# Optimization experiments

Hardware: AMD Instinct MI355X
Metric: run time of the kernel (lower is better)

The kernel has to match this reference:

```python
import jax, jax.numpy as jnp
import numpy as np

D = 1024      # in_features
H = 8         # heads per branch (head_num // 2)
DH = (D // 2) // H  # 64
OUT = 1024

def _split_heads(x, B, S):
    # [B, S, D/2] -> [B, H, S, DH]
    return x.reshape(B, S, H, DH).transpose(0, 2, 1, 3)

def _attn(q, k, v):
    # q,k,v: [B, H, S, DH]
    scores = jnp.einsum('bhqd,bhkd->bhqk', q, k) / jnp.sqrt(jnp.float32(DH))
    a = jax.nn.softmax(scores, axis=-1)
    return jnp.einsum('bhqk,bhkd->bhqd', a, v)

def setup_inputs() -> dict:
    key = jax.random.key(0)
    ks = jax.random.split(key, 16)
    B, S = 2, 2048
    d2 = D // 2
    sc = lambda fan_in: 1.0 / np.sqrt(fan_in)
    inp = {
        'f1': jax.random.normal(ks[0], (B, S, D), jnp.float32),
        'f2': jax.random.normal(ks[1], (B, S, D), jnp.float32),
    }
    names = ['qs', 'ks', 'vs', 'qc', 'kc', 'vc']
    for i, n in enumerate(names):
        inp['W' + n] = jax.random.uniform(ks[2 + i], (d2, D), jnp.float32, -sc(D), sc(D))
        inp['b' + n] = jax.random.uniform(ks[8 + i], (d2,), jnp.float32, -sc(D), sc(D))
    inp['Wo'] = jax.random.uniform(ks[14], (OUT, 2 * D), jnp.float32, -sc(2 * D), sc(2 * D))
    inp['bo'] = jax.random.uniform(ks[15], (OUT,), jnp.float32, -sc(2 * D), sc(2 * D))
    return inp

def reference(f1, f2, Wqs, bqs, Wks, bks, Wvs, bvs, Wqc, bqc, Wkc, bkc, Wvc, bvc, Wo, bo):
    B, S, _ = f1.shape
    lin = lambda x, W, b: jax.nn.relu(x @ W.T + b)
    qs = lin(f1, Wqs, bqs); ks_ = lin(f1, Wks, bks); vs = lin(f1, Wvs, bvs)
    qc = lin(f1, Wqc, bqc); kc = lin(f2, Wkc, bkc); vc = lin(f2, Wvc, bvc)
    ys = _attn(_split_heads(qs, B, S), _split_heads(ks_, B, S), _split_heads(vs, B, S))
    yc = _attn(_split_heads(qc, B, S), _split_heads(kc, B, S), _split_heads(vc, B, S))
    merge = lambda y: y.transpose(0, 2, 1, 3).reshape(B, S, D // 2)
    # reshape_to_batches followed by reshape_from_batches on vs/vc is identity
    y = jnp.concatenate([merge(ys), merge(yc), vs, vc], axis=-1)  # [B, S, 2D]
    return jax.nn.relu(y @ Wo.T + bo)
```

## Files before the change

kernel.cpp:

```cpp
#include <hip/hip_runtime.h>
#include <hip/hip_bf16.h>

using bf16 = __hip_bfloat16;
typedef __attribute__((ext_vector_type(8))) short bf16x8;
typedef __attribute__((ext_vector_type(4))) float f32x4;
typedef __attribute__((ext_vector_type(16))) float f32x16;
typedef __attribute__((ext_vector_type(4))) unsigned int u32x4;

#define MTOT 4096

__device__ __forceinline__ f32x4 fzero() {
    f32x4 z = {0.f, 0.f, 0.f, 0.f};
    return z;
}
__device__ __forceinline__ f32x16 fzero16() {
    f32x16 z = {0.f,0.f,0.f,0.f,0.f,0.f,0.f,0.f,0.f,0.f,0.f,0.f,0.f,0.f,0.f,0.f};
    return z;
}

__device__ __forceinline__ f32x4 mfma16(bf16x8 a, bf16x8 b, f32x4 c) {
    return __builtin_amdgcn_mfma_f32_16x16x32_bf16(a, b, c, 0, 0, 0);
}
__device__ __forceinline__ f32x16 mfma32(bf16x8 a, bf16x8 b, f32x16 c) {
    return __builtin_amdgcn_mfma_f32_32x32x16_bf16(a, b, c, 0, 0, 0);
}

typedef const __attribute__((address_space(1))) unsigned int* gas_ptr;
typedef __attribute__((address_space(3))) unsigned int* las_ptr;
__device__ __forceinline__ void async_copy16(const bf16* g, bf16* l) {
    __builtin_amdgcn_global_load_lds((gas_ptr)(const void*)g, (las_ptr)(void*)l, 16, 0, 0);
}

__device__ __forceinline__ bf16x8 load8(const bf16* p) {
    return *(const bf16x8*)p;
}
__device__ __forceinline__ bf16x8 load8(const float* p) {
    float4 a = *(const float4*)p;
    float4 b = *(const float4*)(p + 4);
    bf16 t[8];
    t[0] = __float2bfloat16(a.x); t[1] = __float2bfloat16(a.y);
    t[2] = __float2bfloat16(a.z); t[3] = __float2bfloat16(a.w);
    t[4] = __float2bfloat16(b.x); t[5] = __float2bfloat16(b.y);
    t[6] = __float2bfloat16(b.z); t[7] = __float2bfloat16(b.w);
    return *(const bf16x8*)t;
}

__device__ __forceinline__ void store_out(bf16* C, size_t idx, float v) {
    C[idx] = __float2bfloat16(v);
}
__device__ __forceinline__ void store_out(float* C, size_t idx, float v) {
    C[idx] = v;
}

__global__ void MultiHeadSelfCrossAttention_7834020348638_kernel(float* out, int n) {
    int i = blockIdx.x * blockDim.x + threadIdx.x;
    if (i < n) out[i] = 0.25f;
}

struct CvtArgs {
    const float* src[9];
    bf16* dst[9];
    int n8[9];
};
__global__ void cvt_kernel(CvtArgs a) {
    int seg = blockIdx.y;
    int t = blockIdx.x * blockDim.x + threadIdx.x;
    if (t < a.n8[seg])
        *(bf16x8*)(a.dst[seg] + (size_t)t * 8) = load8(a.src[seg] + (size_t)t * 8);
}

template <int BN, typename TC>
__device__ __forceinline__ void gemm_fast(
    const bf16* __restrict__ A, int lda,
    const bf16* __restrict__ Bt, int ldb,
    const float* __restrict__ bias,
    TC* __restrict__ C, int ldc,
    int K, int m0, int n0)
{
    constexpr int NI  = BN / 32;
    constexpr int ACH = 128 * 64 / 8 / 256;
    constexpr int BCH = BN * 64 / 8 / 256;

    __shared__ bf16 As[128 * 64];
    __shared__ bf16 Bs[BN * 64];

    const int tid  = threadIdx.x;
    const int lane = tid & 63;
    const int l15  = lane & 15, quad = lane >> 4;
    const int wave = tid >> 6;
    const int wr   = wave >> 1, wc = wave & 1;

    f32x4 acc[4][NI];
#pragma unroll
    for (int mi = 0; mi < 4; mi++)
#pragma unroll
        for (int ni = 0; ni < NI; ni++)
            acc[mi][ni] = fzero();

    for (int k0 = 0; k0 < K; k0 += 64) {
        __syncthreads();
#pragma unroll
        for (int i = 0; i < ACH; i++) {
            int idx = i * 256 + tid;
            int r   = idx >> 3;
            int cg  = (idx & 7) * 8;
            async_copy16(A + (size_t)(m0 + r) * lda + k0 + cg, &As[idx * 8]);
        }
#pragma unroll
        for (int i = 0; i < BCH; i++) {
            int idx = i * 256 + tid;
            int r   = idx >> 3;
            int cg  = (idx & 7) * 8;
            async_copy16(Bt + (size_t)(n0 + r) * ldb + k0 + cg, &Bs[idx * 8]);
        }
        __syncthreads();

#pragma unroll
        for (int ks = 0; ks < 2; ks++) {
            bf16x8 af[4], bfr[NI];
#pragma unroll
            for (int mi = 0; mi < 4; mi++)
                af[mi] = *(const bf16x8*)&As[(wr * 64 + mi * 16 + l15) * 64 + ks * 32 + quad * 8];
#pragma unroll
            for (int ni = 0; ni < NI; ni++)
                bfr[ni] = *(const bf16x8*)&Bs[(wc * (BN / 2) + ni * 16 + l15) * 64 + ks * 32 + quad * 8];
#pragma unroll
            for (int mi = 0; mi < 4; mi++)
#pragma unroll
                for (int ni = 0; ni < NI; ni++)
                    acc[mi][ni] = mfma16(af[mi], bfr[ni], acc[mi][ni]);
        }
    }

#pragma unroll
    for (int ni = 0; ni < NI; ni++) {
        int col = n0 + wc * (BN / 2) + ni * 16 + l15;
        float bb = bias[col];
#pragma unroll
        for (int mi = 0; mi < 4; mi++) {
#pragma unroll
            for (int r = 0; r < 4; r++) {
                int row = m0 + wr * 64 + mi * 16 + quad * 4 + r;
                store_out(C, (size_t)row * ldc + col, fmaxf(acc[mi][ni][r] + bb, 0.f));
            }
        }
    }
}

template <int BN, typename TA, typename TB, typename TC>
__device__ __forceinline__ void gemm_reg(
    const TA* __restrict__ A, int lda,
    const TB* __restrict__ Bt, int ldb,
    const float* __restrict__ bias,
    TC* __restrict__ C, int ldc,
    int K, int m0, int n0)
{
    constexpr int NI  = BN / 32;
    constexpr int BCH = BN * 4 / 256;

    __shared__ bf16 As[128 * 32];
    __shared__ bf16 Bs[BN * 32];

    const int tid  = threadIdx.x;
    const int lane = tid & 63;
    const int l15  = lane & 15, quad = lane >> 4;
    const int wave = tid >> 6;
    const int wr   = wave >> 1, wc = wave & 1;

    f32x4 acc[4][NI];
#pragma unroll
    for (int mi = 0; mi < 4; mi++)
#pragma unroll
        for (int ni = 0; ni < NI; ni++)
            acc[mi][ni] = fzero();

    for (int k0 = 0; k0 < K; k0 += 32) {
        bf16x8 ra[2], rb[BCH];
#pragma unroll
        for (int i = 0; i < 2; i++) {
            int idx = i * 256 + tid;
            ra[i] = load8(A + (size_t)(m0 + (idx >> 2)) * lda + k0 + (idx & 3) * 8);
        }
#pragma unroll
        for (int i = 0; i < BCH; i++) {
            int idx = i * 256 + tid;
            rb[i] = load8(Bt + (size_t)(n0 + (idx >> 2)) * ldb + k0 + (idx & 3) * 8);
        }
        __syncthreads();
#pragma unroll
        for (int i = 0; i < 2; i++)
            *(bf16x8*)&As[(i * 256 + tid) * 8] = ra[i];
#pragma unroll
        for (int i = 0; i < BCH; i++)
            *(bf16x8*)&Bs[(i * 256 + tid) * 8] = rb[i];
        __syncthreads();

        bf16x8 af[4], bfr[NI];
#pragma unroll
        for (int mi = 0; mi < 4; mi++)
            af[mi] = *(const bf16x8*)&As[(wr * 64 + mi * 16 + l15) * 32 + quad * 8];
#pragma unroll
        for (int ni = 0; ni < NI; ni++)
            bfr[ni] = *(const bf16x8*)&Bs[(wc * (BN / 2) + ni * 16 + l15) * 32 + quad * 8];
#pragma unroll
        for (int mi = 0; mi < 4; mi++)
#pragma unroll
            for (int ni = 0; ni < NI; ni++)
                acc[mi][ni] = mfma16(af[mi], bfr[ni], acc[mi][ni]);
    }

#pragma unroll
    for (int ni = 0; ni < NI; ni++) {
        int col = n0 + wc * (BN / 2) + ni * 16 + l15;
        float bb = bias[col];
#pragma unroll
        for (int mi = 0; mi < 4; mi++) {
#pragma unroll
            for (int r = 0; r < 4; r++) {
                int row = m0 + wr * 64 + mi * 16 + quad * 4 + r;
                store_out(C, (size_t)row * ldc + col, fmaxf(acc[mi][ni][r] + bb, 0.f));
            }
        }
    }
}

__global__ void proj_fast(
    const bf16* __restrict__ F1, const bf16* __restrict__ F2,
    const bf16* __restrict__ Wb,
    const float* __restrict__ bqs, const float* __restrict__ bks,
    const float* __restrict__ bvs, const float* __restrict__ bqc,
    const float* __restrict__ bkc, const float* __restrict__ bvc,
    bf16* __restrict__ Y, bf16* Qs, bf16* Ks, bf16* Qc, bf16* Kc)
{
    const int g = blockIdx.z;
    const bf16* X; const float* bi; bf16* C; int ldc;
    switch (g) {
        case 0:  X = F1; bi = bqs; C = Qs;       ldc = 512;  break;
        case 1:  X = F1; bi = bks; C = Ks;       ldc = 512;  break;
        case 2:  X = F1; bi = bvs; C = Y + 1024; ldc = 2048; break;
        case 3:  X = F1; bi = bqc; C = Qc;       ldc = 512;  break;
        case 4:  X = F2; bi = bkc; C = Kc;       ldc = 512;  break;
        default: X = F2; bi = bvc; C = Y + 1536; ldc = 2048; break;
    }
    gemm_fast<128, bf16>(X, 1024, Wb + (size_t)g * 512 * 1024, 1024, bi, C, ldc,
                         1024, blockIdx.y * 128, blockIdx.x * 128);
}

__global__ void out_fast(const bf16* __restrict__ Y, const bf16* __restrict__ WoB,
                         const float* __restrict__ bo, float* __restrict__ out)
{
    gemm_fast<64, float>(Y, 2048, WoB, 2048, bo, out, 1024, 2048,
                         blockIdx.y * 128, blockIdx.x * 64);
}

__global__ void proj_reg(
    const float* __restrict__ f1, const float* __restrict__ f2,
    const float* __restrict__ Wqs, const float* __restrict__ bqs,
    const float* __restrict__ Wks, const float* __restrict__ bks,
    const float* __restrict__ Wvs, const float* __restrict__ bvs,
    const float* __restrict__ Wqc, const float* __restrict__ bqc,
    const float* __restrict__ Wkc, const float* __restrict__ bkc,
    const float* __restrict__ Wvc, const float* __restrict__ bvc,
    bf16* __restrict__ Y, bf16* Qs, bf16* Ks, bf16* Qc, bf16* Kc)
{
    const int g = blockIdx.z;
    const float *X, *W, *bi; bf16* C; int ldc;
    switch (g) {
        case 0:  X = f1; W = Wqs; bi = bqs; C = Qs;       ldc = 512;  break;
        case 1:  X = f1; W = Wks; bi = bks; C = Ks;       ldc = 512;  break;
        case 2:  X = f1; W = Wvs; bi = bvs; C = Y + 1024; ldc = 2048; break;
        case 3:  X = f1; W = Wqc; bi = bqc; C = Qc;       ldc = 512;  break;
        case 4:  X = f2; W = Wkc; bi = bkc; C = Kc;       ldc = 512;  break;
        default: X = f2; W = Wvc; bi = bvc; C = Y + 1536; ldc = 2048; break;
    }
    gemm_reg<128>(X, 1024, W, 1024, bi, C, ldc, 1024, blockIdx.y * 128, blockIdx.x * 128);
}

__global__ void out_reg(const bf16* __restrict__ Y, const float* __restrict__ Wo,
                        const float* __restrict__ bo, float* __restrict__ out)
{
    gemm_reg<64>(Y, 2048, Wo, 2048, bo, out, 1024, 2048, blockIdx.y * 128, blockIdx.x * 64);
}

__global__ void vt_kernel(const bf16* __restrict__ Y, bf16* __restrict__ VT) {
    const int tid = threadIdx.x;
    const int st = blockIdx.x, bh = blockIdx.y, br = blockIdx.z;
    const int b = bh >> 3, h = bh & 7;
    const bf16* src = Y + (size_t)b * 2048 * 2048 + 1024 + br * 512 + h * 64;
    bf16* dst = VT + ((size_t)((br * 2 + b) * 8 + h)) * 64 * 2048;
    const int s0 = st * 64;
#pragma unroll
    for (int i = 0; i < 2; i++) {
        int idx = i * 256 + tid;
        int d = idx >> 3, cs = (idx & 7) * 8;
        bf16 tmp[8];
#pragma unroll
        for (int j = 0; j < 8; j++)
            tmp[j] = src[(size_t)(s0 + cs + j) * 2048 + d];
        *(bf16x8*)&dst[(size_t)d * 2048 + s0 + cs] = *(const bf16x8*)tmp;
    }
}

__global__ __launch_bounds__(256, 2) void attn2_kernel(
    const bf16* __restrict__ Qsb, const bf16* __restrict__ Ksb,
    const bf16* __restrict__ Qcb, const bf16* __restrict__ Kcb,
    const bf16* __restrict__ VT, bf16* __restrict__ Y)
{
    __shared__ bf16 Kbuf[2][64 * 64];
    __shared__ bf16 Vbuf[2][64 * 64];
    __shared__ bf16 QP[128 * 72];

    const int tid  = threadIdx.x;
    const int lane = tid & 63;
    const int l31  = lane & 31;
    const int hi   = lane >> 5;
    const int wave = tid >> 6;

    const int lid   = blockIdx.x + 16 * blockIdx.y + 256 * blockIdx.z;
    const int xcd   = lid & 7, slot = lid >> 3;
    const int combo = xcd + 8 * (slot >> 4);
    const int qt    = slot & 15;
    const int bh    = combo & 15, br = combo >> 4;
    const int b = bh >> 3, h = bh & 7;

    const bf16* Qb = (br ? Qcb : Qsb) + (size_t)b * 2048 * 512 + h * 64;
    const bf16* Kb = (br ? Kcb : Ksb) + (size_t)b * 2048 * 512 + h * 64;
    const bf16* Vt = VT + ((size_t)((br * 2 + b) * 8 + h)) * 64 * 2048;
    bf16*       Ob = Y + (size_t)b * 2048 * 2048 + br * 512 + h * 64;
    const int q0 = qt * 128;

#pragma unroll
    for (int i = 0; i < 4; i++) {
        int idx = i * 256 + tid;
        int r = idx >> 3, c0 = (idx & 7) * 8;
        *(bf16x8*)&QP[r * 72 + c0] = *(const bf16x8*)&Qb[(size_t)(q0 + r) * 512 + c0];
    }

#pragma unroll
    for (int i = 0; i < 2; i++) {
        int idx = i * 256 + tid;
        int r = idx >> 3, sl = (idx & 7) ^ (r & 7);
        async_copy16(Kb + (size_t)r * 512 + sl * 8, &Kbuf[0][idx * 8]);
    }
#pragma unroll
    for (int i = 0; i < 2; i++) {
        int idx = i * 256 + tid;
        int r = idx >> 3, sl = (idx & 7) ^ (r & 7);
        async_copy16(Vt + (size_t)r * 2048 + sl * 8, &Vbuf[0][idx * 8]);
    }
    __syncthreads();

    bf16x8 qf[4];
#pragma unroll
    for (int kq = 0; kq < 4; kq++)
        qf[kq] = *(const bf16x8*)&QP[(wave * 32 + l31) * 72 + kq * 16 + hi * 8];

    const short one_bits = (l31 == 0) ? (short)0x3F80 : (short)0;
    bf16x8 onesA;
#pragma unroll
    for (int j = 0; j < 8; j++) onesA[j] = one_bits;

    f32x16 o[2], ol;
    o[0] = fzero16(); o[1] = fzero16(); ol = fzero16();

    for (int jt = 0; jt < 32; jt++) {
        const int cur = jt & 1;

        if (jt < 31) {
            const size_t s0n = (size_t)(jt + 1) * 64;
#pragma unroll
            for (int i = 0; i < 2; i++) {
                int idx = i * 256 + tid;
                int r = idx >> 3, sl = (idx & 7) ^ (r & 7);
                async_copy16(Kb + (s0n + r) * 512 + sl * 8, &Kbuf[cur ^ 1][idx * 8]);
            }
#pragma unroll
            for (int i = 0; i < 2; i++) {
                int idx = i * 256 + tid;
                int r = idx >> 3, sl = (idx & 7) ^ (r & 7);
                async_copy16(Vt + (size_t)r * 2048 + s0n + sl * 8, &Vbuf[cur ^ 1][idx * 8]);
            }
        }

        f32x16 st[2];
        st[0] = fzero16(); st[1] = fzero16();
#pragma unroll
        for (int t = 0; t < 2; t++)
#pragma unroll
            for (int kq = 0; kq < 4; kq++) {
                bf16x8 kf = *(const bf16x8*)&Kbuf[cur][(t * 32 + l31) * 64
                               + (((kq * 2 + hi) ^ (l31 & 7)) * 8)];
                st[t] = mfma32(kf, qf[kq], st[t]);
            }

        unsigned int pk[2][4][2];
#pragma unroll
        for (int t = 0; t < 2; t++)
#pragma unroll
            for (int g = 0; g < 4; g++) {
                float e0 = __expf(st[t][4 * g + 0] * 0.125f - 4.0f);
                float e1 = __expf(st[t][4 * g + 1] * 0.125f - 4.0f);
                float e2 = __expf(st[t][4 * g + 2] * 0.125f - 4.0f);
                float e3 = __expf(st[t][4 * g + 3] * 0.125f - 4.0f);
                asm("v_cvt_pk_bf16_f32 %0, %1, %2"
                    : "=v"(pk[t][g][0]) : "v"(e0), "v"(e1));
                asm("v_cvt_pk_bf16_f32 %0, %1, %2"
                    : "=v"(pk[t][g][1]) : "v"(e2), "v"(e3));
            }

#pragma unroll
        for (int kb = 0; kb < 4; kb++) {
            const int t = kb >> 1, gb = (kb & 1) * 2;
            unsigned int u0 = pk[t][gb][0],     u1 = pk[t][gb][1];
            unsigned int v0 = pk[t][gb + 1][0], v1 = pk[t][gb + 1][1];
            asm("v_permlane32_swap_b32 %0, %1" : "+v"(u0), "+v"(v0));
            asm("v_permlane32_swap_b32 %0, %1" : "+v"(u1), "+v"(v1));
            u32x4 pw; pw.x = u0; pw.y = u1; pw.z = v0; pw.w = v1;
            bf16x8 pfrag = __builtin_bit_cast(bf16x8, pw);
#pragma unroll
            for (int dt = 0; dt < 2; dt++) {
                bf16x8 vf = *(const bf16x8*)&Vbuf[cur][(dt * 32 + l31) * 64
                               + (((kb * 2 + hi) ^ (l31 & 7)) * 8)];
                o[dt] = mfma32(vf, pfrag, o[dt]);
            }
            ol = mfma32(onesA, pfrag, ol);
        }

        __syncthreads();
    }

    const float linv = 1.0f / __shfl(ol[0], l31);
#pragma unroll
    for (int dt = 0; dt < 2; dt++)
#pragma unroll
        for (int r = 0; r < 16; r++) {
            int d = dt * 32 + (r & 3) + 8 * (r >> 2) + 4 * hi;
            QP[(wave * 32 + l31) * 72 + d] = __float2bfloat16(o[dt][r] * linv);
        }
    __syncthreads();
#pragma unroll
    for (int i = 0; i < 4; i++) {
        int idx = i * 256 + tid;
        int r = idx >> 3, c0 = (idx & 7) * 8;
        *(bf16x8*)&Ob[(size_t)(q0 + r) * 2048 + c0] = *(const bf16x8*)&QP[r * 72 + c0];
    }
}

__global__ __launch_bounds__(256, 4) void attn_kernel(
    const bf16* __restrict__ Qsb, const bf16* __restrict__ Ksb,
    const bf16* __restrict__ Qcb, const bf16* __restrict__ Kcb,
    bf16* __restrict__ Y)
{
    __shared__ bf16 QP[64 * 72];
    __shared__ bf16 Ksh[64 * 72];
    __shared__ bf16 Vsh[64 * 72];

    const int tid  = threadIdx.x;
    const int lane = tid & 63;
    const int l15  = lane & 15, quad = lane >> 4;
    const int wave = tid >> 6;
    const int qt = blockIdx.x, bh = blockIdx.y, br = blockIdx.z;
    const int b = bh >> 3, h = bh & 7;

    const bf16* Qb = (br ? Qcb : Qsb) + (size_t)b * 2048 * 512 + h * 64;
    const bf16* Kb = (br ? Kcb : Ksb) + (size_t)b * 2048 * 512 + h * 64;
    const bf16* Vb = Y + (size_t)b * 2048 * 2048 + 1024 + br * 512 + h * 64;
    bf16*       Ob = Y + (size_t)b * 2048 * 2048 +        br * 512 + h * 64;
    const int q0 = qt * 64;

#pragma unroll
    for (int i = 0; i < 2; i++) {
        int idx = i * 256 + tid;
        int r = idx >> 3, c0 = (idx & 7) * 8;
        *(bf16x8*)&QP[r * 72 + c0] = *(const bf16x8*)&Qb[(size_t)(q0 + r) * 512 + c0];
    }
    __syncthreads();

    bf16x8 qf[2];
#pragma unroll
    for (int ks = 0; ks < 2; ks++)
        qf[ks] = *(const bf16x8*)&QP[(wave * 16 + l15) * 72 + ks * 32 + quad * 8];

    const short one_bits = l15 == 0 ? (short)0x3F80 : (short)0;
    bf16x8 onesf;
#pragma unroll
    for (int j = 0; j < 8; j++) onesf[j] = one_bits;

    f32x4 o[4], o_l;
    o_l = fzero();
#pragma unroll
    for (int ni = 0; ni < 4; ni++) o[ni] = fzero();

    const int kr0 = tid >> 3, kc0 = (tid & 7) * 8;
    const int kr1 = (256 + tid) >> 3;

    bf16x8 kr[2], vr[2];
    kr[0] = *(const bf16x8*)&Kb[(size_t)kr0 * 512 + kc0];
    kr[1] = *(const bf16x8*)&Kb[(size_t)kr1 * 512 + kc0];
    vr[0] = *(const bf16x8*)&Vb[(size_t)lane * 2048 + (0 * 4 + wave) * 8];
    vr[1] = *(const bf16x8*)&Vb[(size_t)lane * 2048 + (1 * 4 + wave) * 8];

    for (int jt = 0; jt < 32; jt++) {
        __syncthreads();
        *(bf16x8*)&Ksh[kr0 * 72 + kc0] = kr[0];
        *(bf16x8*)&Ksh[kr1 * 72 + kc0] = kr[1];
#pragma unroll
        for (int i = 0; i < 2; i++) {
            int cg = i * 4 + wave;
            const bf16* e = (const bf16*)&vr[i];
#pragma unroll
            for (int j = 0; j < 8; j++)
                Vsh[(cg * 8 + j) * 72 + lane] = e[j];
        }
        __syncthreads();

        {
            const int s0n = (jt < 31) ? (jt + 1) * 64 : 31 * 64;
            kr[0] = *(const bf16x8*)&Kb[(size_t)(s0n + kr0) * 512 + kc0];
            kr[1] = *(const bf16x8*)&Kb[(size_t)(s0n + kr1) * 512 + kc0];
            vr[0] = *(const bf16x8*)&Vb[(size_t)(s0n + lane) * 2048 + (0 * 4 + wave) * 8];
            vr[1] = *(const bf16x8*)&Vb[(size_t)(s0n + lane) * 2048 + (1 * 4 + wave) * 8];
        }

        f32x4 s[4];
#pragma unroll
        for (int ni = 0; ni < 4; ni++) s[ni] = fzero();
#pragma unroll
        for (int ni = 0; ni < 4; ni++)
#pragma unroll
            for (int ks = 0; ks < 2; ks++) {
                bf16x8 kf = *(const bf16x8*)&Ksh[(ni * 16 + l15) * 72 + ks * 32 + quad * 8];
                s[ni] = mfma16(qf[ks], kf, s[ni]);
            }

#pragma unroll
        for (int ni = 0; ni < 4; ni++)
#pragma unroll
            for (int r = 0; r < 4; r++) {
                float p = __expf(s[ni][r] * 0.125f - 4.0f);
                QP[(wave * 16 + quad * 4 + r) * 72 + ni * 16 + l15] = __float2bfloat16(p);
            }

#pragma unroll
        for (int ks = 0; ks < 2; ks++) {
            bf16x8 pf = *(const bf16x8*)&QP[(wave * 16 + l15) * 72 + ks * 32 + quad * 8];
#pragma unroll
            for (int ni = 0; ni < 4; ni++) {
                bf16x8 vf = *(const bf16x8*)&Vsh[(ni * 16 + l15) * 72 + ks * 32 + quad * 8];
                o[ni] = mfma16(pf, vf, o[ni]);
            }
            o_l = mfma16(pf, onesf, o_l);
        }
    }

#pragma unroll
    for (int r = 0; r < 4; r++) {
        float lsum = __shfl(o_l[r], quad << 4);
        float inv = 1.f / lsum;
        int row = q0 + wave * 16 + quad * 4 + r;
#pragma unroll
        for (int ni = 0; ni < 4; ni++)
            Ob[(size_t)row * 2048 + ni * 16 + l15] = __float2bfloat16(o[ni][r] * inv);
    }
}

extern "C" void kernel_launch(void* const* d_in, const int* in_sizes, int n_in,
                              void* d_out, int out_size, void* d_ws, size_t ws_size,
                              hipStream_t stream) {
    const size_t out_bytes = (size_t)out_size * sizeof(float);
    const size_t ws_base = ((size_t)MTOT * 2048 + 4 * (size_t)MTOT * 512) * 2;
    const size_t ws_fast = ws_base + ((size_t)2 * MTOT * 1024 + 6 * 512 * 1024 + 1024 * 2048) * 2;
    const size_t vt_elems = (size_t)2 * 2 * 8 * 64 * 2048;
    const size_t ws_fast2 = ws_fast + vt_elems * 2;

    if (n_in != 16) { hipMemsetAsync(d_out, 0x43, out_bytes, stream); return; }
    if (ws_size < ws_base) { hipMemsetAsync(d_out, 0x41, out_bytes, stream); return; }

    const float* f1  = (const float*)d_in[0];
    const float* f2  = (const float*)d_in[1];
    const float* Wqs = (const float*)d_in[2];  const float* bqs = (const float*)d_in[3];
    const float* Wks = (const float*)d_in[4];  const float* bks = (const float*)d_in[5];
    const float* Wvs = (const float*)d_in[6];  const float* bvs = (const float*)d_in[7];
    const float* Wqc = (const float*)d_in[8];  const float* bqc = (const float*)d_in[9];
    const float* Wkc = (const float*)d_in[10]; const float* bkc = (const float*)d_in[11];
    const float* Wvc = (const float*)d_in[12]; const float* bvc = (const float*)d_in[13];
    const float* Wo  = (const float*)d_in[14]; const float* bo  = (const float*)d_in[15];

    bf16* Y  = (bf16*)d_ws;
    bf16* Qs = Y  + (size_t)MTOT * 2048;
    bf16* Ks = Qs + (size_t)MTOT * 512;
    bf16* Qc = Ks + (size_t)MTOT * 512;
    bf16* Kc = Qc + (size_t)MTOT * 512;
    float* out = (float*)d_out;

    if (ws_size >= ws_fast) {
        bf16* F1  = Kc + (size_t)MTOT * 512;
        bf16* F2  = F1 + (size_t)MTOT * 1024;
        bf16* Wb  = F2 + (size_t)MTOT * 1024;
        bf16* WoB = Wb + (size_t)6 * 512 * 1024;
        bf16* VT  = WoB + (size_t)1024 * 2048;

        CvtArgs ca;
        ca.src[0] = f1;  ca.dst[0] = F1;  ca.n8[0] = MTOT * 1024 / 8;
        ca.src[1] = f2;  ca.dst[1] = F2;  ca.n8[1] = MTOT * 1024 / 8;
        const float* ws_[6] = {Wqs, Wks, Wvs, Wqc, Wkc, Wvc};
        for (int i = 0; i < 6; i++) {
            ca.src[2 + i] = ws_[i];
            ca.dst[2 + i] = Wb + (size_t)i * 512 * 1024;
            ca.n8[2 + i]  = 512 * 1024 / 8;
        }
        ca.src[8] = Wo; ca.dst[8] = WoB; ca.n8[8] = 1024 * 2048 / 8;

        cvt_kernel<<<dim3((MTOT * 1024 / 8 + 255) / 256, 9), 256, 0, stream>>>(ca);
        proj_fast<<<dim3(4, 32, 6), 256, 0, stream>>>(
            F1, F2, Wb, bqs, bks, bvs, bqc, bkc, bvc, Y, Qs, Ks, Qc, Kc);
        if (ws_size >= ws_fast2) {
            vt_kernel<<<dim3(32, 16, 2), 256, 0, stream>>>(Y, VT);
            attn2_kernel<<<dim3(16, 16, 2), 256, 0, stream>>>(Qs, Ks, Qc, Kc, VT, Y);
        } else {
            attn_kernel<<<dim3(32, 16, 2), 256, 0, stream>>>(Qs, Ks, Qc, Kc, Y);
        }
        out_fast<<<dim3(16, 32), 256, 0, stream>>>(Y, WoB, bo, out);
    } else {
        proj_reg<<<dim3(4, 32, 6), 256, 0, stream>>>(
            f1, f2, Wqs, bqs, Wks, bks, Wvs, bvs, Wqc, bqc, Wkc, bkc, Wvc, bvc,
            Y, Qs, Ks, Qc, Kc);
        attn_kernel<<<dim3(32, 16, 2), 256, 0, stream>>>(Qs, Ks, Qc, Kc, Y);
        out_reg<<<dim3(16, 32), 256, 0, stream>>>(Y, Wo, bo, out);
    }
}
```

Before: 244.6 us.

## Alias Q staging into K/V buffers, raise occupancy, use raw exp2 and setprio

The attention kernel now reuses one 32 KB shared buffer for the Q staging area and the double-buffered K/V tiles. Q fragments are read into registers before the K/V prefetch overwrites that region. This lowers LDS use so launch bounds can request 4 blocks per SM instead of 2. The exponent is computed with a single fma plus a raw v_exp_f32, with the scale and constant shift folded into base-2 constants, and s_setprio is raised around the MFMA sections so matrix work is favoured across waves. The risks are register pressure under the tighter launch bound and a small change in exp accuracy.

```diff
diff --git a/kernel.cpp b/kernel.cpp
--- a/kernel.cpp
+++ b/kernel.cpp
@@ -23,6 +23,12 @@
 }
 __device__ __forceinline__ f32x16 mfma32(bf16x8 a, bf16x8 b, f32x16 c) {
     return __builtin_amdgcn_mfma_f32_32x32x16_bf16(a, b, c, 0, 0, 0);
+}
+
+__device__ __forceinline__ float exp2_raw(float x) {
+    float r;
+    asm("v_exp_f32 %0, %1" : "=v"(r) : "v"(x));
+    return r;
 }
 
 typedef const __attribute__((address_space(1))) unsigned int* gas_ptr;
@@ -301,14 +307,12 @@
     }
 }
 
-__global__ __launch_bounds__(256, 2) void attn2_kernel(
+__global__ __launch_bounds__(256, 4) void attn2_kernel(
     const bf16* __restrict__ Qsb, const bf16* __restrict__ Ksb,
     const bf16* __restrict__ Qcb, const bf16* __restrict__ Kcb,
     const bf16* __restrict__ VT, bf16* __restrict__ Y)
 {
-    __shared__ bf16 Kbuf[2][64 * 64];
-    __shared__ bf16 Vbuf[2][64 * 64];
-    __shared__ bf16 QP[128 * 72];
+    __shared__ bf16 SMEM[4][64 * 64];
 
     const int tid  = threadIdx.x;
     const int lane = tid & 63;
@@ -329,31 +333,35 @@
     bf16*       Ob = Y + (size_t)b * 2048 * 2048 + br * 512 + h * 64;
     const int q0 = qt * 128;
 
+    bf16* QP = &SMEM[0][0];
+
 #pragma unroll
     for (int i = 0; i < 4; i++) {
         int idx = i * 256 + tid;
         int r = idx >> 3, c0 = (idx & 7) * 8;
         *(bf16x8*)&QP[r * 72 + c0] = *(const bf16x8*)&Qb[(size_t)(q0 + r) * 512 + c0];
     }
+    __syncthreads();
+
+    bf16x8 qf[4];
+#pragma unroll
+    for (int kq = 0; kq < 4; kq++)
+        qf[kq] = *(const bf16x8*)&QP[(wave * 32 + l31) * 72 + kq * 16 + hi * 8];
+    __syncthreads();
 
 #pragma unroll
     for (int i = 0; i < 2; i++) {
         int idx = i * 256 + tid;
         int r = idx >> 3, sl = (idx & 7) ^ (r & 7);
-        async_copy16(Kb + (size_t)r * 512 + sl * 8, &Kbuf[0][idx * 8]);
+        async_copy16(Kb + (size_t)r * 512 + sl * 8, &SMEM[0][idx * 8]);
     }
 #pragma unroll
     for (int i = 0; i < 2; i++) {
         int idx = i * 256 + tid;
         int r = idx >> 3, sl = (idx & 7) ^ (r & 7);
-        async_copy16(Vt + (size_t)r * 2048 + sl * 8, &Vbuf[0][idx * 8]);
+        async_copy16(Vt + (size_t)r * 2048 + sl * 8, &SMEM[1][idx * 8]);
     }
     __syncthreads();
-
-    bf16x8 qf[4];
-#pragma unroll
-    for (int kq = 0; kq < 4; kq++)
-        qf[kq] = *(const bf16x8*)&QP[(wave * 32 + l31) * 72 + kq * 16 + hi * 8];
 
     const short one_bits = (l31 == 0) ? (short)0x3F80 : (short)0;
     bf16x8 onesA;
@@ -363,51 +371,61 @@
     f32x16 o[2], ol;
     o[0] = fzero16(); o[1] = fzero16(); ol = fzero16();
 
+    const float C1 = 0.18033688011112043f;
+    const float C2 = -5.7707801635558535f;
+
     for (int jt = 0; jt < 32; jt++) {
         const int cur = jt & 1;
+        const bf16* Kc = &SMEM[cur * 2][0];
+        const bf16* Vc = &SMEM[cur * 2 + 1][0];
 
         if (jt < 31) {
             const size_t s0n = (size_t)(jt + 1) * 64;
+            bf16* Kn = &SMEM[(cur ^ 1) * 2][0];
+            bf16* Vn = &SMEM[(cur ^ 1) * 2 + 1][0];
 #pragma unroll
             for (int i = 0; i < 2; i++) {
                 int idx = i * 256 + tid;
                 int r = idx >> 3, sl = (idx & 7) ^ (r & 7);
-                async_copy16(Kb + (s0n + r) * 512 + sl * 8, &Kbuf[cur ^ 1][idx * 8]);
+                async_copy16(Kb + (s0n + r) * 512 + sl * 8, &Kn[idx * 8]);
             }
 #pragma unroll
             for (int i = 0; i < 2; i++) {
                 int idx = i * 256 + tid;
                 int r = idx >> 3, sl = (idx & 7) ^ (r & 7);
-                async_copy16(Vt + (size_t)r * 2048 + s0n + sl * 8, &Vbuf[cur ^ 1][idx * 8]);
+                async_copy16(Vt + (size_t)r * 2048 + s0n + sl * 8, &Vn[idx * 8]);
             }
         }
 
         f32x16 st[2];
         st[0] = fzero16(); st[1] = fzero16();
+        __builtin_amdgcn_s_setprio(1);
 #pragma unroll
         for (int t = 0; t < 2; t++)
 #pragma unroll
             for (int kq = 0; kq < 4; kq++) {
-                bf16x8 kf = *(const bf16x8*)&Kbuf[cur][(t * 32 + l31) * 64
+                bf16x8 kf = *(const bf16x8*)&Kc[(t * 32 + l31) * 64
                                + (((kq * 2 + hi) ^ (l31 & 7)) * 8)];
                 st[t] = mfma32(kf, qf[kq], st[t]);
             }
+        __builtin_amdgcn_s_setprio(0);
 
         unsigned int pk[2][4][2];
 #pragma unroll
         for (int t = 0; t < 2; t++)
 #pragma unroll
             for (int g = 0; g < 4; g++) {
-                float e0 = __expf(st[t][4 * g + 0] * 0.125f - 4.0f);
-                float e1 = __expf(st[t][4 * g + 1] * 0.125f - 4.0f);
-                float e2 = __expf(st[t][4 * g + 2] * 0.125f - 4.0f);
-                float e3 = __expf(st[t][4 * g + 3] * 0.125f - 4.0f);
+                float e0 = exp2_raw(fmaf(st[t][4 * g + 0], C1, C2));
+                float e1 = exp2_raw(fmaf(st[t][4 * g + 1], C1, C2));
+                float e2 = exp2_raw(fmaf(st[t][4 * g + 2], C1, C2));
+                float e3 = exp2_raw(fmaf(st[t][4 * g + 3], C1, C2));
                 asm("v_cvt_pk_bf16_f32 %0, %1, %2"
                     : "=v"(pk[t][g][0]) : "v"(e0), "v"(e1));
                 asm("v_cvt_pk_bf16_f32 %0, %1, %2"
                     : "=v"(pk[t][g][1]) : "v"(e2), "v"(e3));
             }
 
+        __builtin_amdgcn_s_setprio(1);
 #pragma unroll
         for (int kb = 0; kb < 4; kb++) {
             const int t = kb >> 1, gb = (kb & 1) * 2;
@@ -419,12 +437,13 @@
             bf16x8 pfrag = __builtin_bit_cast(bf16x8, pw);
 #pragma unroll
             for (int dt = 0; dt < 2; dt++) {
-                bf16x8 vf = *(const bf16x8*)&Vbuf[cur][(dt * 32 + l31) * 64
+                bf16x8 vf = *(const bf16x8*)&Vc[(dt * 32 + l31) * 64
                                + (((kb * 2 + hi) ^ (l31 & 7)) * 8)];
                 o[dt] = mfma32(vf, pfrag, o[dt]);
             }
             ol = mfma32(onesA, pfrag, ol);
         }
+        __builtin_amdgcn_s_setprio(0);
 
         __syncthreads();
     }
```

Result: faster. 233.3 us (-4.6%).
